# Kernel optimization log

Measured on AMD Instinct MI355X. Metric: run time of the kernel, lower is better.

## Reference

```python
import jax, jax.numpy as jnp
import numpy as np


def setup_inputs() -> dict:
    key = jax.random.key(0)
    k1, k2, k3 = jax.random.split(key, 3)
    B, N, F, U = 8, 2048, 128, 128
    A = jax.random.uniform(k1, (B, N, N), dtype=jnp.float32)   # dense nonneg adjacency
    X = jax.random.normal(k2, (B, N, F), dtype=jnp.float32)
    W = jax.random.normal(k3, (F, U), dtype=jnp.float32)
    bias = jnp.zeros((U,), dtype=jnp.float32)
    p = jnp.zeros((1,), dtype=jnp.float32)
    q = jnp.zeros((1,), dtype=jnp.float32)
    return {"A": A, "X": X, "W": W, "bias": bias, "p": p, "q": q}


def reference(A, X, W, bias, p, q):
    # learn_pqr path of MyGCN: A_ = D @ (A + q*I) @ D with D = diag(k^-0.25),
    # k = p + (1-p)*colsum(A). Diag matmuls expressed as broadcasted scaling (same math).
    B, N, _ = A.shape
    ps = jax.nn.sigmoid(p)          # shape (1,)
    qs = jax.nn.sigmoid(q)
    Dr = jnp.sum(A, axis=1)          # [B, N]  (K.sum axis=1)
    k_vec = ps + (1.0 - ps) * Dr     # [B, N]
    k_inv_root = jnp.sqrt(k_vec) ** -0.5   # k^{-0.25}
    k_clean = jnp.where(jnp.isinf(k_inv_root), 0.0, k_inv_root)  # [B, N]
    I = jnp.eye(N, dtype=A.dtype)
    AqI = A + qs[0] * I              # [B, N, N]
    A_ = k_clean[:, :, None] * AqI * k_clean[:, None, :]
    XW = jnp.einsum('bnf,fu->bnu', X, W)        # [B, N, U]
    A_XW = jnp.einsum('bnm,bmu->bnu', A_, XW)   # [B, N, U]
    out = A_XW + bias
    return jax.nn.relu(out)
```

## Files before the change

### kernel.cpp

```cpp
#include <hip/hip_runtime.h>
#include <stdint.h>

#define N 2048
#define F 128
#define UDIM 128

typedef __attribute__((ext_vector_type(8))) __bf16 bf16x8;
typedef __attribute__((ext_vector_type(8))) unsigned short us8;
typedef __attribute__((ext_vector_type(4))) float f32x4;

__device__ __forceinline__ unsigned short f2bf(float f) {
  union { float f; uint32_t u; } v; v.f = f;
  uint32_t u = v.u;
  return (unsigned short)((u + 0x7FFFu + ((u >> 16) & 1u)) >> 16);
}
__device__ __forceinline__ float bf2f(unsigned short u) {
  union { uint32_t u; float f; } v; v.u = ((uint32_t)u) << 16; return v.f;
}
__device__ __forceinline__ uint32_t cvtpk(float lo, float hi) {
  uint32_t r;
  asm("v_cvt_pk_bf16_f32 %0, %1, %2" : "=v"(r) : "v"(lo), "v"(hi));
  return r;
}

__device__ __forceinline__ void async_load16(const void* g, void* l) {
  typedef const __attribute__((address_space(1))) uint32_t* gp_t;
  typedef __attribute__((address_space(3))) uint32_t* lp_t;
  __builtin_amdgcn_global_load_lds((gp_t)(uintptr_t)g, (lp_t)(uint32_t)(uintptr_t)l, 16, 0, 0);
}

__global__ __launch_bounds__(256, 4)
void gcn_pass1(const float* __restrict__ A, const float* __restrict__ X,
               const float* __restrict__ W, float* __restrict__ partial,
               unsigned short* __restrict__ Z) {
  __shared__ __align__(16) unsigned short Wl[128 * 128];
  __shared__ __align__(16) unsigned short Xl[32 * 128];

  const int bid = blockIdx.x;
  const int t = threadIdx.x;

  if (bid < 1024) {
    const int b = bid >> 7;
    const int rc = (bid >> 1) & 63;
    const int j = (bid & 1) * 1024 + t * 4;
    const float* ap = A + (size_t)b * N * N + (size_t)rc * 32 * N + j;
    float s0 = 0.f, s1 = 0.f, s2 = 0.f, s3 = 0.f;
    #pragma unroll 4
    for (int rr = 0; rr < 32; ++rr) {
      float4 v = *(const float4*)(ap + (size_t)rr * N);
      s0 += v.x; s1 += v.y; s2 += v.z; s3 += v.w;
    }
    float4 s; s.x = s0; s.y = s1; s.z = s2; s.w = s3;
    *(float4*)&partial[((size_t)b * 64 + rc) * N + j] = s;
    return;
  }

  const int zid = bid - 1024;
  const int lane = t & 63;
  const int wid = t >> 6;
  const int b = zid >> 6;
  const int i0 = (zid & 63) << 5;

  {
    const int u = t & 127;
    const int khalf = t >> 7;
    #pragma unroll
    for (int g = 0; g < 8; ++g) {
      const int k0 = khalf * 64 + g * 8;
      float v[8];
      #pragma unroll
      for (int e = 0; e < 8; ++e) v[e] = W[(size_t)(k0 + e) * 128 + u];
      uint4 w;
      w.x = cvtpk(v[0], v[1]); w.y = cvtpk(v[2], v[3]);
      w.z = cvtpk(v[4], v[5]); w.w = cvtpk(v[6], v[7]);
      const int slot = khalf * 8 + g;
      *(uint4*)&Wl[u * 128 + ((slot ^ (u & 7)) * 8)] = w;
    }
  }
  {
    const int r = t >> 3;
    const float* xp = X + ((size_t)b * N + i0 + r) * F + (t & 7) * 8;
    #pragma unroll
    for (int h = 0; h < 2; ++h) {
      float4 v0 = *(const float4*)(xp + h * 64);
      float4 v1 = *(const float4*)(xp + h * 64 + 4);
      uint4 w;
      w.x = cvtpk(v0.x, v0.y); w.y = cvtpk(v0.z, v0.w);
      w.z = cvtpk(v1.x, v1.y); w.w = cvtpk(v1.z, v1.w);
      const int slot = (t & 7) + h * 8;
      *(uint4*)&Xl[r * 128 + ((slot ^ (r & 7)) * 8)] = w;
    }
  }
  __syncthreads();

  f32x4 acc[2][2];
  #pragma unroll
  for (int a = 0; a < 2; ++a)
    #pragma unroll
    for (int c = 0; c < 2; ++c) { f32x4 z = {0.f, 0.f, 0.f, 0.f}; acc[a][c] = z; }

  const int u0 = wid * 32;
  #pragma unroll
  for (int kc = 0; kc < 4; ++kc) {
    bf16x8 af[2], bfv[2];
    #pragma unroll
    for (int ut = 0; ut < 2; ++ut) {
      const int u = u0 + ut * 16 + (lane & 15);
      const int sl = ((kc * 4 + (lane >> 4)) ^ (u & 7)) * 8;
      af[ut] = *(const bf16x8*)&Wl[u * 128 + sl];
    }
    #pragma unroll
    for (int it = 0; it < 2; ++it) {
      const int rr = it * 16 + (lane & 15);
      const int sl = ((kc * 4 + (lane >> 4)) ^ (rr & 7)) * 8;
      bfv[it] = *(const bf16x8*)&Xl[rr * 128 + sl];
    }
    #pragma unroll
    for (int ut = 0; ut < 2; ++ut)
      #pragma unroll
      for (int it = 0; it < 2; ++it)
        acc[ut][it] = __builtin_amdgcn_mfma_f32_16x16x32_bf16(af[ut], bfv[it], acc[ut][it], 0, 0, 0);
  }

  #pragma unroll
  for (int ut = 0; ut < 2; ++ut)
    #pragma unroll
    for (int it = 0; it < 2; ++it) {
      const int ic = i0 + it * 16 + (lane & 15);
      #pragma unroll
      for (int rg = 0; rg < 4; ++rg) {
        const int u = u0 + ut * 16 + (lane >> 4) * 4 + rg;
        Z[((size_t)b * UDIM + u) * N + ic] = f2bf(acc[ut][it][rg]);
      }
    }
}

__global__ __launch_bounds__(256, 4)
void gcn_scale(const float* __restrict__ partial, const float* __restrict__ pptr,
               const unsigned short* __restrict__ Z, float* __restrict__ kcl,
               unsigned short* __restrict__ YT) {
  __shared__ float red[2][128];
  __shared__ float kct[128];
  const int t = threadIdx.x;
  const int b = blockIdx.x >> 4;
  const int ic = (blockIdx.x & 15) * 128;

  {
    const int i = ic + (t & 127);
    const int half = t >> 7;
    float s = 0.f;
    #pragma unroll 8
    for (int rc = half * 32; rc < half * 32 + 32; ++rc)
      s += partial[((size_t)b * 64 + rc) * N + i];
    red[half][t & 127] = s;
  }
  __syncthreads();
  if (t < 128) {
    const float s = red[0][t] + red[1][t];
    const float sp = 1.0f / (1.0f + __expf(-pptr[0]));
    const float k = sp + (1.0f - sp) * s;
    float rv = rsqrtf(sqrtf(k));
    if (isinf(rv)) rv = 0.f;
    kct[t] = rv;
    kcl[b * N + ic + t] = rv;
  }
  __syncthreads();

  const int i8 = (t & 15) * 8;
  #pragma unroll
  for (int it = 0; it < 8; ++it) {
    const int u = it * 16 + (t >> 4);
    const size_t off = ((size_t)b * UDIM + u) * N + ic + i8;
    us8 z = *(const us8*)&Z[off];
    float y[8];
    #pragma unroll
    for (int e = 0; e < 8; ++e) y[e] = bf2f(z[e]) * kct[i8 + e];
    uint4 w;
    w.x = cvtpk(y[0], y[1]); w.y = cvtpk(y[2], y[3]);
    w.z = cvtpk(y[4], y[5]); w.w = cvtpk(y[6], y[7]);
    *(uint4*)&YT[off] = w;
  }
}

__global__ __launch_bounds__(256, 2)
void gcn_gemm(const float* __restrict__ A, const unsigned short* __restrict__ YT,
              const float* __restrict__ kcl, const float* __restrict__ bias,
              const float* __restrict__ qptr, float* __restrict__ out) {
  __shared__ __align__(16) unsigned short Abuf[4 * 32 * 64];
  __shared__ __align__(16) unsigned short Ybuf[4 * 128 * 64];

  const int t = threadIdx.x;
  const int lane = t & 63;
  const int wid = t >> 6;
  const int wr = wid >> 1;
  const int wc = wid & 1;

  const int bid = blockIdx.x;
  const int b = bid & 7;
  const int i0 = (bid >> 3) << 5;

  const float qs = 1.0f / (1.0f + __expf(-qptr[0]));

  const int r = t >> 3;
  const int c8 = t & 7;
  const float* Ap = A + (size_t)b * N * N + (size_t)(i0 + r) * N + c8 * 8;
  const unsigned short* YTb = YT + (size_t)b * UDIM * N;

  const int a_woff = r * 64 + ((c8 ^ (r & 7)) * 8);
  const int y_u = t >> 3;
  const int y_wavebase = (t & ~63) * 8;

  f32x4 acc[4];
  #pragma unroll
  for (int i = 0; i < 4; ++i) { f32x4 z = {0.f, 0.f, 0.f, 0.f}; acc[i] = z; }

  float4 a0A, a1A, a0B, a1B;

  auto issueY = [&](int kt, int buf) {
    const int k0 = kt * 64;
    #pragma unroll
    for (int rnd = 0; rnd < 4; ++rnd) {
      const int u = rnd * 32 + y_u;
      const int c16 = (t & 7) ^ (u & 7);
      async_load16(YTb + (size_t)u * N + k0 + c16 * 8, &Ybuf[buf * 8192 + rnd * 2048 + y_wavebase]);
    }
  };
  auto compute = [&](int cur) {
    const unsigned short* Ac = Abuf + cur * 2048;
    const unsigned short* Yc = Ybuf + cur * 8192;
    #pragma unroll
    for (int kk = 0; kk < 2; ++kk) {
      const int ar = 16 * wr + (lane & 15);
      const int as = ((kk * 4 + (lane >> 4)) ^ (ar & 7)) * 8;
      bf16x8 af = *(const bf16x8*)&Ac[ar * 64 + as];
      #pragma unroll
      for (int ut = 0; ut < 4; ++ut) {
        const int u = 64 * wc + ut * 16 + (lane & 15);
        const int bs = ((kk * 4 + (lane >> 4)) ^ (u & 7)) * 8;
        bf16x8 bfv = *(const bf16x8*)&Yc[u * 64 + bs];
        acc[ut] = __builtin_amdgcn_mfma_f32_16x16x32_bf16(af, bfv, acc[ut], 0, 0, 0);
      }
    }
  };

#define SB __builtin_amdgcn_sched_barrier(0)
#define ISSUE_A(KT, R0, R1) { R0 = *(const float4*)(Ap + (KT) * 64); R1 = *(const float4*)(Ap + (KT) * 64 + 4); }
#define CVT_A(BUF, R0, R1) { \
    uint4 w; w.x = cvtpk(R0.x, R0.y); w.y = cvtpk(R0.z, R0.w); \
    w.z = cvtpk(R1.x, R1.y); w.w = cvtpk(R1.z, R1.w); \
    *(uint4*)&Abuf[(BUF) * 2048 + a_woff] = w; }

  ISSUE_A(0, a0A, a1A); SB;
  ISSUE_A(1, a0B, a1B); SB;
  issueY(0, 0); SB;
  asm volatile("s_waitcnt vmcnt(6)" ::: "memory");
  CVT_A(0, a0A, a1A); SB;
  ISSUE_A(2, a0A, a1A); SB;
  issueY(1, 1); SB;
  asm volatile("s_waitcnt vmcnt(10)" ::: "memory");
  CVT_A(1, a0B, a1B); SB;
  ISSUE_A(3, a0B, a1B); SB;
  issueY(2, 2); SB;

#define GSTEP(KT, VM, R0, R1, DO_A, DO_Y)                          \
  {                                                                \
    asm volatile("s_waitcnt vmcnt(" #VM ")" ::: "memory");         \
    CVT_A(((KT) + 2) & 3, R0, R1);                                 \
    asm volatile("s_waitcnt lgkmcnt(0)" ::: "memory");             \
    __builtin_amdgcn_s_barrier(); SB;                              \
    if (DO_A) { ISSUE_A((KT) + 4, R0, R1); } SB;                   \
    if (DO_Y) { issueY((KT) + 3, ((KT) + 3) & 3); } SB;            \
    __builtin_amdgcn_s_setprio(1);                                 \
    compute((KT) & 3);                                             \
    __builtin_amdgcn_s_setprio(0); SB;                             \
  }

  #pragma unroll 1
  for (int kt = 0; kt < 28; kt += 2) {
    GSTEP(kt, 10, a0A, a1A, true, true);
    GSTEP(kt + 1, 10, a0B, a1B, true, true);
  }
  GSTEP(28, 10, a0A, a1A, false, true);
  GSTEP(29, 8, a0B, a1B, false, false);
  asm volatile("s_waitcnt vmcnt(4)" ::: "memory");
  __builtin_amdgcn_s_barrier(); SB;
  compute(2);
  asm volatile("s_waitcnt vmcnt(0)" ::: "memory");
  __builtin_amdgcn_s_barrier(); SB;
  compute(3);
#undef GSTEP
#undef CVT_A
#undef ISSUE_A
#undef SB

  const int irow = i0 + 16 * wr + (lane >> 4) * 4;
  #pragma unroll
  for (int ut = 0; ut < 4; ++ut) {
    const int u = 64 * wc + ut * 16 + (lane & 15);
    const float bv = bias[u];
    #pragma unroll
    for (int rg = 0; rg < 4; ++rg) {
      const int i = irow + rg;
      const float yv = bf2f(YTb[(size_t)u * N + i]);
      const float kv = kcl[b * N + i];
      float vv = kv * (acc[ut][rg] + qs * yv) + bv;
      out[((size_t)b * N + i) * UDIM + u] = vv > 0.f ? vv : 0.f;
    }
  }
}

extern "C" void kernel_launch(void* const* d_in, const int* in_sizes, int n_in,
                              void* d_out, int out_size, void* d_ws, size_t ws_size,
                              hipStream_t stream) {
  (void)in_sizes; (void)n_in; (void)out_size; (void)ws_size;
  const float* A    = (const float*)d_in[0];
  const float* X    = (const float*)d_in[1];
  const float* W    = (const float*)d_in[2];
  const float* bias = (const float*)d_in[3];
  const float* p    = (const float*)d_in[4];
  const float* q    = (const float*)d_in[5];
  float* out = (float*)d_out;

  char* ws = (char*)d_ws;
  float* partial      = (float*)ws;
  float* kcl          = (float*)(ws + 4194304);
  unsigned short* Zb  = (unsigned short*)(ws + 4259840);
  unsigned short* YT  = (unsigned short*)(ws + 8454144);

  gcn_pass1<<<dim3(1536), dim3(256), 0, stream>>>(A, X, W, partial, Zb);
  gcn_scale<<<dim3(128), dim3(256), 0, stream>>>(partial, p, Zb, kcl, YT);
  gcn_gemm<<<dim3(512), dim3(256), 0, stream>>>(A, YT, kcl, bias, q, out);
}
```

Measured before the change: 58.86 us.

## Fold column scaling into GEMM A-tile conversion and drop the scale kernel

Removes the separate scale kernel. The last colsum block per batch, chosen with an atomic ticket counter, computes the k^-1/4 scale vector. The GEMM stages kcl in LDS, applies the column scale to A while converting it to bf16, and uses Z directly instead of a pre-scaled YT. To fit the extra kcs LDS array, the GEMM pipeline drops from 4 to 3 stages. This saves one launch and one full read/write pass over Z, at the cost of extra multiplies in the A conversion, a memset launch, a shallower prefetch, and a serialized reduction inside one block per batch.

```diff
diff --git a/kernel.cpp b/kernel.cpp
--- a/kernel.cpp
+++ b/kernel.cpp
@@ -22,7 +22,6 @@
   asm("v_cvt_pk_bf16_f32 %0, %1, %2" : "=v"(r) : "v"(lo), "v"(hi));
   return r;
 }
-
 __device__ __forceinline__ void async_load16(const void* g, void* l) {
   typedef const __attribute__((address_space(1))) uint32_t* gp_t;
   typedef __attribute__((address_space(3))) uint32_t* lp_t;
@@ -31,10 +30,10 @@
 
 __global__ __launch_bounds__(256, 4)
 void gcn_pass1(const float* __restrict__ A, const float* __restrict__ X,
-               const float* __restrict__ W, float* __restrict__ partial,
-               unsigned short* __restrict__ Z) {
-  __shared__ __align__(16) unsigned short Wl[128 * 128];
-  __shared__ __align__(16) unsigned short Xl[32 * 128];
+               const float* __restrict__ W, const float* __restrict__ pptr,
+               float* __restrict__ partial, unsigned short* __restrict__ Z,
+               float* __restrict__ kcl, unsigned int* __restrict__ tickets) {
+  __shared__ __align__(16) unsigned char LDSRAW[40960];
 
   const int bid = blockIdx.x;
   const int t = threadIdx.x;
@@ -52,6 +51,31 @@
     }
     float4 s; s.x = s0; s.y = s1; s.z = s2; s.w = s3;
     *(float4*)&partial[((size_t)b * 64 + rc) * N + j] = s;
+
+    unsigned int* lf = (unsigned int*)LDSRAW;
+    __threadfence();
+    __syncthreads();
+    if (t == 0) {
+      const unsigned int old = atomicAdd(&tickets[b * 32], 1u);
+      *lf = (old == 127u) ? 1u : 0u;
+    }
+    __syncthreads();
+    if (*lf) {
+      __threadfence();
+      const float sp = 1.0f / (1.0f + __expf(-pptr[0]));
+      #pragma unroll 1
+      for (int kq = 0; kq < 8; ++kq) {
+        const int jj = kq * 256 + t;
+        float s = 0.f;
+        #pragma unroll 4
+        for (int rc2 = 0; rc2 < 64; ++rc2)
+          s += partial[((size_t)b * 64 + rc2) * N + jj];
+        const float k = sp + (1.0f - sp) * s;
+        float rv = rsqrtf(sqrtf(k));
+        if (isinf(rv)) rv = 0.f;
+        kcl[b * N + jj] = rv;
+      }
+    }
     return;
   }
 
@@ -60,6 +84,8 @@
   const int wid = t >> 6;
   const int b = zid >> 6;
   const int i0 = (zid & 63) << 5;
+  unsigned short* Wl = (unsigned short*)LDSRAW;
+  unsigned short* Xl = (unsigned short*)(LDSRAW + 32768);
 
   {
     const int u = t & 127;
@@ -135,59 +161,13 @@
     }
 }
 
-__global__ __launch_bounds__(256, 4)
-void gcn_scale(const float* __restrict__ partial, const float* __restrict__ pptr,
-               const unsigned short* __restrict__ Z, float* __restrict__ kcl,
-               unsigned short* __restrict__ YT) {
-  __shared__ float red[2][128];
-  __shared__ float kct[128];
-  const int t = threadIdx.x;
-  const int b = blockIdx.x >> 4;
-  const int ic = (blockIdx.x & 15) * 128;
-
-  {
-    const int i = ic + (t & 127);
-    const int half = t >> 7;
-    float s = 0.f;
-    #pragma unroll 8
-    for (int rc = half * 32; rc < half * 32 + 32; ++rc)
-      s += partial[((size_t)b * 64 + rc) * N + i];
-    red[half][t & 127] = s;
-  }
-  __syncthreads();
-  if (t < 128) {
-    const float s = red[0][t] + red[1][t];
-    const float sp = 1.0f / (1.0f + __expf(-pptr[0]));
-    const float k = sp + (1.0f - sp) * s;
-    float rv = rsqrtf(sqrtf(k));
-    if (isinf(rv)) rv = 0.f;
-    kct[t] = rv;
-    kcl[b * N + ic + t] = rv;
-  }
-  __syncthreads();
-
-  const int i8 = (t & 15) * 8;
-  #pragma unroll
-  for (int it = 0; it < 8; ++it) {
-    const int u = it * 16 + (t >> 4);
-    const size_t off = ((size_t)b * UDIM + u) * N + ic + i8;
-    us8 z = *(const us8*)&Z[off];
-    float y[8];
-    #pragma unroll
-    for (int e = 0; e < 8; ++e) y[e] = bf2f(z[e]) * kct[i8 + e];
-    uint4 w;
-    w.x = cvtpk(y[0], y[1]); w.y = cvtpk(y[2], y[3]);
-    w.z = cvtpk(y[4], y[5]); w.w = cvtpk(y[6], y[7]);
-    *(uint4*)&YT[off] = w;
-  }
-}
-
 __global__ __launch_bounds__(256, 2)
-void gcn_gemm(const float* __restrict__ A, const unsigned short* __restrict__ YT,
+void gcn_gemm(const float* __restrict__ A, const unsigned short* __restrict__ Z,
               const float* __restrict__ kcl, const float* __restrict__ bias,
               const float* __restrict__ qptr, float* __restrict__ out) {
-  __shared__ __align__(16) unsigned short Abuf[4 * 32 * 64];
-  __shared__ __align__(16) unsigned short Ybuf[4 * 128 * 64];
+  __shared__ __align__(16) unsigned short Abuf[3 * 32 * 64];
+  __shared__ __align__(16) unsigned short Ybuf[3 * 128 * 64];
+  __shared__ __align__(16) float kcs[2048];
 
   const int t = threadIdx.x;
   const int lane = t & 63;
@@ -204,12 +184,20 @@
   const int r = t >> 3;
   const int c8 = t & 7;
   const float* Ap = A + (size_t)b * N * N + (size_t)(i0 + r) * N + c8 * 8;
-  const unsigned short* YTb = YT + (size_t)b * UDIM * N;
+  const unsigned short* Zb = Z + (size_t)b * UDIM * N;
 
   const int a_woff = r * 64 + ((c8 ^ (r & 7)) * 8);
   const int y_u = t >> 3;
   const int y_wavebase = (t & ~63) * 8;
 
+  {
+    float4 v0 = *(const float4*)&kcl[b * N + t * 8];
+    float4 v1 = *(const float4*)&kcl[b * N + t * 8 + 4];
+    *(float4*)&kcs[t * 8] = v0;
+    *(float4*)&kcs[t * 8 + 4] = v1;
+  }
+  __syncthreads();
+
   f32x4 acc[4];
   #pragma unroll
   for (int i = 0; i < 4; ++i) { f32x4 z = {0.f, 0.f, 0.f, 0.f}; acc[i] = z; }
@@ -222,7 +210,7 @@
     for (int rnd = 0; rnd < 4; ++rnd) {
       const int u = rnd * 32 + y_u;
       const int c16 = (t & 7) ^ (u & 7);
-      async_load16(YTb + (size_t)u * N + k0 + c16 * 8, &Ybuf[buf * 8192 + rnd * 2048 + y_wavebase]);
+      async_load16(Zb + (size_t)u * N + k0 + c16 * 8, &Ybuf[buf * 8192 + rnd * 2048 + y_wavebase]);
     }
   };
   auto compute = [&](int cur) {
@@ -245,49 +233,54 @@
 
 #define SB __builtin_amdgcn_sched_barrier(0)
 #define ISSUE_A(KT, R0, R1) { R0 = *(const float4*)(Ap + (KT) * 64); R1 = *(const float4*)(Ap + (KT) * 64 + 4); }
-#define CVT_A(BUF, R0, R1) { \
-    uint4 w; w.x = cvtpk(R0.x, R0.y); w.y = cvtpk(R0.z, R0.w); \
-    w.z = cvtpk(R1.x, R1.y); w.w = cvtpk(R1.z, R1.w); \
+#define CVT_A(BUF, R0, R1, K0) { \
+    float4 kj0 = *(const float4*)&kcs[(K0) + c8 * 8]; \
+    float4 kj1 = *(const float4*)&kcs[(K0) + c8 * 8 + 4]; \
+    uint4 w; \
+    w.x = cvtpk(R0.x * kj0.x, R0.y * kj0.y); \
+    w.y = cvtpk(R0.z * kj0.z, R0.w * kj0.w); \
+    w.z = cvtpk(R1.x * kj1.x, R1.y * kj1.y); \
+    w.w = cvtpk(R1.z * kj1.z, R1.w * kj1.w); \
     *(uint4*)&Abuf[(BUF) * 2048 + a_woff] = w; }
+
+  asm volatile("s_waitcnt vmcnt(0) lgkmcnt(0)" ::: "memory");
 
   ISSUE_A(0, a0A, a1A); SB;
   ISSUE_A(1, a0B, a1B); SB;
   issueY(0, 0); SB;
   asm volatile("s_waitcnt vmcnt(6)" ::: "memory");
-  CVT_A(0, a0A, a1A); SB;
+  CVT_A(0, a0A, a1A, 0); SB;
   ISSUE_A(2, a0A, a1A); SB;
   issueY(1, 1); SB;
-  asm volatile("s_waitcnt vmcnt(10)" ::: "memory");
-  CVT_A(1, a0B, a1B); SB;
-  ISSUE_A(3, a0B, a1B); SB;
-  issueY(2, 2); SB;
 
 #define GSTEP(KT, VM, R0, R1, DO_A, DO_Y)                          \
   {                                                                \
     asm volatile("s_waitcnt vmcnt(" #VM ")" ::: "memory");         \
-    CVT_A(((KT) + 2) & 3, R0, R1);                                 \
+    CVT_A(((KT) + 1) % 3, R0, R1, ((KT) + 1) * 64);                \
     asm volatile("s_waitcnt lgkmcnt(0)" ::: "memory");             \
     __builtin_amdgcn_s_barrier(); SB;                              \
-    if (DO_A) { ISSUE_A((KT) + 4, R0, R1); } SB;                   \
-    if (DO_Y) { issueY((KT) + 3, ((KT) + 3) & 3); } SB;            \
+    if (DO_A) { ISSUE_A((KT) + 3, R0, R1); } SB;                   \
+    if (DO_Y) { issueY((KT) + 2, ((KT) + 2) % 3); } SB;            \
     __builtin_amdgcn_s_setprio(1);                                 \
-    compute((KT) & 3);                                             \
+    compute((KT) % 3);                                             \
     __builtin_amdgcn_s_setprio(0); SB;                             \
   }
 
   #pragma unroll 1
   for (int kt = 0; kt < 28; kt += 2) {
-    GSTEP(kt, 10, a0A, a1A, true, true);
-    GSTEP(kt + 1, 10, a0B, a1B, true, true);
-  }
-  GSTEP(28, 10, a0A, a1A, false, true);
-  GSTEP(29, 8, a0B, a1B, false, false);
+    GSTEP(kt,     6, a0B, a1B, true, true);
+    GSTEP(kt + 1, 6, a0A, a1A, true, true);
+  }
+  GSTEP(28, 6, a0B, a1B, true, true);
+  GSTEP(29, 6, a0A, a1A, false, true);
   asm volatile("s_waitcnt vmcnt(4)" ::: "memory");
+  CVT_A(1, a0B, a1B, 31 * 64);
+  asm volatile("s_waitcnt lgkmcnt(0)" ::: "memory");
   __builtin_amdgcn_s_barrier(); SB;
-  compute(2);
+  compute(0);
   asm volatile("s_waitcnt vmcnt(0)" ::: "memory");
   __builtin_amdgcn_s_barrier(); SB;
-  compute(3);
+  compute(1);
 #undef GSTEP
 #undef CVT_A
 #undef ISSUE_A
@@ -301,9 +294,9 @@
     #pragma unroll
     for (int rg = 0; rg < 4; ++rg) {
       const int i = irow + rg;
-      const float yv = bf2f(YTb[(size_t)u * N + i]);
-      const float kv = kcl[b * N + i];
-      float vv = kv * (acc[ut][rg] + qs * yv) + bv;
+      const float zv = bf2f(Zb[(size_t)u * N + i]);
+      const float kv = kcs[i];
+      float vv = kv * acc[ut][rg] + qs * kv * kv * zv + bv;
       out[((size_t)b * N + i) * UDIM + u] = vv > 0.f ? vv : 0.f;
     }
   }
@@ -322,12 +315,12 @@
   float* out = (float*)d_out;
 
   char* ws = (char*)d_ws;
-  float* partial      = (float*)ws;
-  float* kcl          = (float*)(ws + 4194304);
-  unsigned short* Zb  = (unsigned short*)(ws + 4259840);
-  unsigned short* YT  = (unsigned short*)(ws + 8454144);
-
-  gcn_pass1<<<dim3(1536), dim3(256), 0, stream>>>(A, X, W, partial, Zb);
-  gcn_scale<<<dim3(128), dim3(256), 0, stream>>>(partial, p, Zb, kcl, YT);
-  gcn_gemm<<<dim3(512), dim3(256), 0, stream>>>(A, YT, kcl, bias, q, out);
-}
+  unsigned int* tickets = (unsigned int*)ws;
+  float* partial        = (float*)(ws + 4096);
+  float* kcl            = (float*)(ws + 4096 + 4194304);
+  unsigned short* Zb    = (unsigned short*)(ws + 4096 + 4194304 + 65536);
+
+  hipMemsetAsync(tickets, 0, 1024, stream);
+  gcn_pass1<<<dim3(1536), dim3(256), 0, stream>>>(A, X, W, p, partial, Zb, kcl, tickets);
+  gcn_gemm<<<dim3(512), dim3(256), 0, stream>>>(A, Zb, kcl, bias, q, out);
+}
```

After: 213.7 us. 3.63x slower.
